# Kernel tuning notes

Measured on AMD Instinct MI355X. Metric: run time of the kernel, lower is better.

## Reference

```python
import jax, jax.numpy as jnp
import numpy as np

B, S, D_IN, D_OUT = 4, 2048, 1024, 1024
USE_MASK = True


def setup_inputs() -> dict:
    key = jax.random.key(0)
    ks = jax.random.split(key, 6)
    return {
        "inputs_for_keys": jax.random.normal(ks[0], (B, S, D_IN), jnp.float32),
        "inputs_for_values": jax.random.normal(ks[1], (B, S, D_IN), jnp.float32),
        "inputs_for_queries": jax.random.normal(ks[2], (B, S, D_IN), jnp.float32),
        "WK": jax.random.normal(ks[3], (D_IN, D_OUT), jnp.float32) * 0.1,
        "WV": jax.random.normal(ks[4], (D_IN, D_OUT), jnp.float32) * 0.1,
        "WQ": jax.random.normal(ks[5], (D_IN, D_OUT), jnp.float32) * 0.1,
    }


def reference(inputs_for_keys, inputs_for_values, inputs_for_queries, WK, WV, WQ):
    # projections: [B,S,Din] @ [Din,Dout] -> [B,S,Dout]
    K = jnp.einsum("bsd,de->bse", inputs_for_keys, WK)
    V = jnp.einsum("bsd,de->bse", inputs_for_values, WV)
    Q = jnp.einsum("bsd,de->bse", inputs_for_queries, WQ)

    dk = jnp.asarray(K.shape[2], jnp.float32)
    # scores: [B, Sq, Sk]
    score = jnp.einsum("bqd,bkd->bqk", Q, K) / jnp.sqrt(dk)
    if USE_MASK:
        # causal: -inf strictly above diagonal (j > i), matching the
        # transposed tril(-1) * -inf construction in the original.
        q_idx = jnp.arange(S)[:, None]
        k_idx = jnp.arange(S)[None, :]
        mask = jnp.where(k_idx > q_idx, -jnp.inf, 0.0).astype(score.dtype)
        score = score + mask[None, :, :]
    soft_score = jax.nn.softmax(score, axis=-1)
    return jnp.einsum("bqk,bkd->bqd", soft_score, V)
```

## Files before the change

### kernel.cpp

```cpp
#include <hip/hip_runtime.h>
#include <hip/hip_bf16.h>

typedef unsigned short u16;
typedef _Float16 f16;
typedef __attribute__((ext_vector_type(8))) short s16x8;
typedef __attribute__((ext_vector_type(8))) _Float16 f16x8;
typedef __attribute__((ext_vector_type(4))) float f32x4;
typedef __attribute__((ext_vector_type(4))) unsigned short u16x4;

template <typename T>
__device__ __forceinline__ auto mfma_try(T a, T b, f32x4 c, int)
    -> decltype(__builtin_amdgcn_mfma_f32_16x16x32_f16(a, b, c, 0, 0, 0)) {
  return __builtin_amdgcn_mfma_f32_16x16x32_f16(a, b, c, 0, 0, 0);
}
template <typename T>
__device__ __forceinline__ f32x4 mfma_try(T a, T b, f32x4 c, long) {
  return __builtin_amdgcn_mfma_f32_16x16x32_f16(
      __builtin_bit_cast(f16x8, a), __builtin_bit_cast(f16x8, b), c, 0, 0, 0);
}
__device__ __forceinline__ f32x4 MFMA16(s16x8 a, s16x8 b, f32x4 c) {
  return mfma_try(a, b, c, 0);
}

__device__ __forceinline__ void gload16(const void* g, void* s) {
  __builtin_amdgcn_global_load_lds(
      (const __attribute__((address_space(1))) void*)g,
      (__attribute__((address_space(3))) void*)s, 16, 0, 0);
}

__device__ __forceinline__ u16 f2h(float x) {
  f16 h = (f16)x;
  u16 u;
  __builtin_memcpy(&u, &h, 2);
  return u;
}
__device__ __forceinline__ float h2f(u16 u) {
  f16 h;
  __builtin_memcpy(&h, &u, 2);
  return (float)h;
}

#define LDS_SWZ(r, cb) ((cb) ^ (((r)&7) << 4))

struct Geom {
  int srow[4], scol[4];
  int w, l, wr, wc;
};

__device__ __forceinline__ Geom make_geom() {
  Geom g;
  int tid = threadIdx.x;
  g.w = tid >> 6; g.l = tid & 63;
  g.wr = g.w >> 1; g.wc = g.w & 1;
#pragma unroll
  for (int i = 0; i < 4; ++i) {
    int off = i * 4096 + g.w * 1024 + g.l * 16;
    int r = off >> 7, cb = off & 127;
    g.srow[i] = r;
    g.scol[i] = LDS_SWZ(r, cb) >> 1;
  }
  return g;
}

__device__ __forceinline__ void stage(const u16* pan, int ld, int k0,
                                      char* lds, const Geom& g) {
#pragma unroll
  for (int i = 0; i < 4; ++i)
    gload16(pan + (long)g.srow[i] * ld + k0 + g.scol[i],
            lds + i * 4096 + g.w * 1024);
}

__device__ __forceinline__ void compute_step(const char* lA, const char* lB,
                                             const Geom& g, f32x4 acc[4][4]) {
#pragma unroll
  for (int ks = 0; ks < 2; ++ks) {
    s16x8 af[4], bg[4];
#pragma unroll
    for (int m = 0; m < 4; ++m) {
      int r = g.wr * 64 + m * 16 + (g.l & 15);
      int cb = ks * 64 + ((g.l >> 4) << 4);
      af[m] = *(const s16x8*)(lA + r * 128 + LDS_SWZ(r, cb));
    }
#pragma unroll
    for (int n = 0; n < 4; ++n) {
      int r = g.wc * 64 + n * 16 + (g.l & 15);
      int cb = ks * 64 + ((g.l >> 4) << 4);
      bg[n] = *(const s16x8*)(lB + r * 128 + LDS_SWZ(r, cb));
    }
#pragma unroll
    for (int m = 0; m < 4; ++m)
#pragma unroll
      for (int n = 0; n < 4; ++n)
        acc[m][n] = MFMA16(af[m], bg[n], acc[m][n]);
  }
}

__device__ __forceinline__ void gemm_core(const u16* Apan, int lda,
                                          const u16* Bpan, int ldb, int nsteps,
                                          char* lA, char* lB, const Geom& g,
                                          f32x4 acc[4][4]) {
  stage(Apan, lda, 0, lA, g);
  stage(Bpan, ldb, 0, lB, g);
  __syncthreads();
  for (int t = 0; t < nsteps; ++t) {
    int cur = (t & 1) << 14;
    if (t + 1 < nsteps) {
      int nxt = ((t + 1) & 1) << 14;
      stage(Apan, lda, (t + 1) * 64, lA + nxt, g);
      stage(Bpan, ldb, (t + 1) * 64, lB + nxt, g);
    }
    compute_step(lA + cur, lB + cur, g, acc);
    if (t + 1 < nsteps) __syncthreads();
  }
}

__global__ __launch_bounds__(256, 2) void proj_kernel(
    const u16* __restrict__ xk, const u16* __restrict__ xq, const u16* __restrict__ xv,
    const u16* __restrict__ wk, const u16* __restrict__ wq, const u16* __restrict__ wv,
    u16* __restrict__ K, u16* __restrict__ Q, u16* __restrict__ Vt) {
  __shared__ char lds[65536];
  const int y = blockIdx.y;
  const u16* X = y == 0 ? xk : (y == 1 ? xq : xv);
  const u16* W = y == 0 ? wk : (y == 1 ? wq : wv);
  const int bx = blockIdx.x;
  const int swz = (bx & 7) * 64 + (bx >> 3);
  const int tm = swz >> 3, tn = swz & 7;
  Geom g = make_geom();
  f32x4 acc[4][4] = {};
  gemm_core(X + (long)tm * 128 * 1024, 1024, W + (long)tn * 128 * 1024, 1024,
            16, lds, lds + 32768, g, acc);
  const int rg0 = tm * 128 + g.wr * 64, cg0 = tn * 128 + g.wc * 64;
  if (y < 2) {
    u16* C = y == 0 ? K : Q;
#pragma unroll
    for (int m = 0; m < 4; ++m)
#pragma unroll
      for (int n = 0; n < 4; ++n)
#pragma unroll
        for (int j = 0; j < 4; ++j) {
          int rg = rg0 + m * 16 + ((g.l >> 4) << 2) + j;
          int cg = cg0 + n * 16 + (g.l & 15);
          C[(long)rg * 1024 + cg] = f2h(acc[m][n][j]);
        }
  } else {
#pragma unroll
    for (int m = 0; m < 4; ++m) {
      int rg = rg0 + m * 16 + ((g.l >> 4) << 2);
      int b = rg >> 11, rl = rg & 2047;
#pragma unroll
      for (int n = 0; n < 4; ++n) {
        int cg = cg0 + n * 16 + (g.l & 15);
        u16x4 pk;
#pragma unroll
        for (int j = 0; j < 4; ++j) pk[j] = f2h(acc[m][n][j]);
        *(u16x4*)(Vt + (long)b * (1024 * 2048) + (long)cg * 2048 + rl) = pk;
      }
    }
  }
}

__global__ __launch_bounds__(256, 2) void qkt_kernel(
    const u16* __restrict__ Q, const u16* __restrict__ K, u16* __restrict__ S) {
  __shared__ char lds[65536];
  const int bx = blockIdx.x;
  const int swz = (bx & 7) * 68 + (bx >> 3);
  const int b = swz / 136;
  int t = swz - b * 136;
  int tm = 0;
  while (t > tm) { t -= tm + 1; ++tm; }
  const int tn = t;
  Geom g = make_geom();
  f32x4 acc[4][4] = {};
  const u16* Qb = Q + (long)b * 2048 * 1024;
  const u16* Kb = K + (long)b * 2048 * 1024;
  gemm_core(Qb + (long)tm * 128 * 1024, 1024, Kb + (long)tn * 128 * 1024, 1024,
            16, lds, lds + 32768, g, acc);
  u16* Sb = S + (long)b * 2048 * 2048;
  const int rg0 = tm * 128 + g.wr * 64, cg0 = tn * 128 + g.wc * 64;
#pragma unroll
  for (int m = 0; m < 4; ++m)
#pragma unroll
    for (int n = 0; n < 4; ++n)
#pragma unroll
      for (int j = 0; j < 4; ++j) {
        int rg = rg0 + m * 16 + ((g.l >> 4) << 2) + j;
        int cg = cg0 + n * 16 + (g.l & 15);
        Sb[(long)rg * 2048 + cg] = f2h(acc[m][n][j]);
      }
}

__global__ __launch_bounds__(256, 2) void pv_kernel(
    const u16* __restrict__ P, const u16* __restrict__ Vt, float* __restrict__ O) {
  __shared__ char lds[65536];
  const int bx = blockIdx.x;
  const int swz = (bx & 7) * 64 + (bx >> 3);
  const int b = swz >> 7, loc = swz & 127;
  const int tm = loc >> 3, tn = loc & 7;
  Geom g = make_geom();
  f32x4 acc[4][4] = {};
  gemm_core(P + ((long)b * 2048 + tm * 128) * 2048, 2048,
            Vt + (long)b * 1024 * 2048 + (long)tn * 128 * 2048, 2048,
            (tm + 1) * 2, lds, lds + 32768, g, acc);
  const int rg0 = tm * 128 + g.wr * 64, cg0 = tn * 128 + g.wc * 64;
#pragma unroll
  for (int m = 0; m < 4; ++m)
#pragma unroll
    for (int n = 0; n < 4; ++n)
#pragma unroll
      for (int j = 0; j < 4; ++j) {
        int rg = rg0 + m * 16 + ((g.l >> 4) << 2) + j;
        int cg = cg0 + n * 16 + (g.l & 15);
        O[((long)b * 2048 + rg) * 1024 + cg] = acc[m][n][j];
      }
}

__global__ __launch_bounds__(256) void softmax_causal(
    const u16* __restrict__ S, u16* __restrict__ P) {
  const int row = blockIdx.x;
  const int i_q = row & 2047;
  const u16* sr = S + (long)row * 2048;
  u16* pr = P + (long)row * 2048;
  const int tid = threadIdx.x;
  const int l = tid & 63, w = tid >> 6;
  const int base = tid * 8;

  s16x8 raw = *(const s16x8*)(sr + base);
  float v[8];
  float m = -INFINITY;
#pragma unroll
  for (int j = 0; j < 8; ++j) {
    float x = h2f((u16)raw[j]);
    x = (base + j <= i_q) ? x : -INFINITY;
    v[j] = x;
    m = fmaxf(m, x);
  }
  __shared__ float red[8];
  for (int o = 32; o; o >>= 1) m = fmaxf(m, __shfl_xor(m, o, 64));
  if (l == 0) red[w] = m;
  __syncthreads();
  m = fmaxf(fmaxf(red[0], red[1]), fmaxf(red[2], red[3]));

  float s = 0.f;
#pragma unroll
  for (int j = 0; j < 8; ++j) {
    v[j] = expf(v[j] - m);
    s += v[j];
  }
  for (int o = 32; o; o >>= 1) s += __shfl_xor(s, o, 64);
  if (l == 0) red[4 + w] = s;
  __syncthreads();
  s = (red[4] + red[5]) + (red[6] + red[7]);
  float inv = 1.0f / s;

  s16x8 o;
#pragma unroll
  for (int j = 0; j < 8; ++j) o[j] = (short)f2h(v[j] * inv);
  *(s16x8*)(pr + base) = o;
}

__global__ __launch_bounds__(256) void xcast_kernel(
    const float* __restrict__ x0, const float* __restrict__ x1,
    const float* __restrict__ x2, u16* __restrict__ o0, u16* __restrict__ o1,
    u16* __restrict__ o2) {
  const int y = blockIdx.y;
  const float* in = y == 0 ? x0 : (y == 1 ? x1 : x2);
  u16* out = y == 0 ? o0 : (y == 1 ? o1 : o2);
  long i = ((long)blockIdx.x * 256 + threadIdx.x) * 8;
  f32x4 a = *(const f32x4*)(in + i);
  f32x4 b = *(const f32x4*)(in + i + 4);
  s16x8 o;
#pragma unroll
  for (int j = 0; j < 4; ++j) {
    o[j] = (short)f2h(a[j]);
    o[4 + j] = (short)f2h(b[j]);
  }
  *(s16x8*)(out + i) = o;
}

__global__ __launch_bounds__(256) void wcast_kernel(
    const float* __restrict__ wk, const float* __restrict__ wv,
    const float* __restrict__ wq, u16* __restrict__ ok, u16* __restrict__ ov,
    u16* __restrict__ oq) {
  __shared__ float tile[32][33];
  const int z = blockIdx.z;
  const float* w = z == 0 ? wk : (z == 1 ? wv : wq);
  u16* o = z == 0 ? ok : (z == 1 ? ov : oq);
  const float scale = (z == 2) ? 0.03125f : 1.0f;
  const int bx = blockIdx.x, by = blockIdx.y;
  const int lx = threadIdx.x & 31, ly = threadIdx.x >> 5;
#pragma unroll
  for (int j = 0; j < 32; j += 8)
    tile[ly + j][lx] = w[(long)(by * 32 + ly + j) * 1024 + bx * 32 + lx];
  __syncthreads();
#pragma unroll
  for (int j = 0; j < 32; j += 8)
    o[(long)(bx * 32 + ly + j) * 1024 + by * 32 + lx] = f2h(tile[lx][ly + j] * scale);
}

extern "C" void kernel_launch(void* const* d_in, const int* in_sizes, int n_in,
                              void* d_out, int out_size, void* d_ws, size_t ws_size,
                              hipStream_t stream) {
  const float* Xk = (const float*)d_in[0];
  const float* Xv = (const float*)d_in[1];
  const float* Xq = (const float*)d_in[2];
  const float* WK = (const float*)d_in[3];
  const float* WV = (const float*)d_in[4];
  const float* WQ = (const float*)d_in[5];

  const int Bn = 4, S = 2048, D = 1024;
  const long NX = (long)Bn * S * D;

  const size_t r0 = (size_t)Bn * S * S * 4;
  const size_t r1 = r0 + 3ull * D * D * 2;
  const size_t r2 = r1 + 2ull * NX * 2;
  const size_t NEED = r2 + (size_t)NX * 2;
  if (ws_size < NEED) {
    hipMemsetAsync(d_out, 0, (size_t)out_size * 4, stream);
    return;
  }
  char* ws = (char*)d_ws;
  u16* xkb = (u16*)ws;
  u16* xvb = xkb + NX;
  u16* xqb = xvb + NX;
  u16* scoresH = (u16*)ws;
  u16* wkt = (u16*)(ws + r0);
  u16* wvt = wkt + D * D;
  u16* wqt = wvt + D * D;
  u16* Kb = (u16*)(ws + r1);
  u16* Qb = Kb + NX;
  u16* Pb = (u16*)(ws + r1);
  u16* Vt = (u16*)(ws + r2);

  xcast_kernel<<<dim3(4096, 3), 256, 0, stream>>>(Xk, Xv, Xq, xkb, xvb, xqb);
  wcast_kernel<<<dim3(32, 32, 3), 256, 0, stream>>>(WK, WV, WQ, wkt, wvt, wqt);
  proj_kernel<<<dim3(512, 3), 256, 0, stream>>>(xkb, xqb, xvb, wkt, wqt, wvt,
                                                Kb, Qb, Vt);
  qkt_kernel<<<dim3(544), 256, 0, stream>>>(Qb, Kb, scoresH);
  softmax_causal<<<dim3(8192), 256, 0, stream>>>(scoresH, Pb);
  pv_kernel<<<dim3(512), 256, 0, stream>>>(Pb, Vt, (float*)d_out);
}
```

Baseline: 163.4 us.

## Use 256x256 tiles with 8-wave pipelined GEMM for projection and QK^T

Replaces the 128x128, 4-wave GEMM used by the projection and score kernels with a 256x256 tile, 8-wave core. The new core double-buffers 64 KB LDS stages, splits global-to-LDS loads into halves that are issued between MFMA quarters, and uses explicit waitcnt, barriers and setprio. The goal is higher operand reuse and better overlap of loads with MFMA work. In exchange there are far fewer blocks (144 for QK^T), much larger LDS use, and possible tail or occupancy loss.

After: 171.7 us. 1.05x slower.

```diff
diff --git a/kernel.cpp b/kernel.cpp
--- a/kernel.cpp
+++ b/kernel.cpp
@@ -41,6 +41,183 @@
 }
 
 #define LDS_SWZ(r, cb) ((cb) ^ (((r)&7) << 4))
+
+__device__ __forceinline__ void bar() { __builtin_amdgcn_s_barrier(); }
+__device__ __forceinline__ void lgkm0() {
+  asm volatile("s_waitcnt lgkmcnt(0)" ::: "memory");
+  __builtin_amdgcn_sched_barrier(0);
+}
+__device__ __forceinline__ void vm4() {
+  asm volatile("s_waitcnt vmcnt(4)" ::: "memory");
+}
+__device__ __forceinline__ void vm0() {
+  asm volatile("s_waitcnt vmcnt(0)" ::: "memory");
+}
+
+__device__ __forceinline__ void gemm256_core(
+    const u16* __restrict__ Apan, int lda, const u16* __restrict__ Bpan,
+    int ldb, int ns, char* lds, f32x4 (&acc)[8][4]) {
+  const int tid = threadIdx.x;
+  const int w = tid >> 6, l = tid & 63;
+  const int wr = w >> 2, wc = w & 3;
+
+  const int sr = tid >> 3;
+  const int scol = (((tid & 7) * 16) ^ ((sr & 7) << 4)) >> 1;
+
+  auto stageH = [&](const u16* pan, int ld, int t, int h, int region) {
+    char* dst = lds + ((t & 1) << 16) + region * 16384 + (w << 10);
+    const u16* src = pan + (long)(h * 128 + sr) * ld + t * 64 + scol;
+    gload16(src, dst);
+    gload16(src + (long)64 * ld, dst + 8192);
+  };
+  auto rdA = [&](int p, int m, int ks) -> s16x8 {
+    int r = m * 16 + (l & 15);
+    int cb = ks * 64 + ((l >> 4) << 4);
+    return *(const s16x8*)(lds + (p << 16) + wr * 16384 + r * 128 + LDS_SWZ(r, cb));
+  };
+  auto rdB = [&](int p, int n, int ks) -> s16x8 {
+    int row = wc * 64 + n * 16 + (l & 15);
+    int r = row & 127;
+    int cb = ks * 64 + ((l >> 4) << 4);
+    return *(const s16x8*)(lds + (p << 16) + (2 + (wc >> 1)) * 16384 + r * 128 +
+                           LDS_SWZ(r, cb));
+  };
+
+  stageH(Apan, lda, 0, 0, 0);
+  stageH(Apan, lda, 0, 1, 1);
+  stageH(Bpan, ldb, 0, 0, 2);
+  stageH(Bpan, ldb, 0, 1, 3);
+  if (ns > 1) {
+    stageH(Apan, lda, 1, 0, 0);
+    stageH(Apan, lda, 1, 1, 1);
+    vm4();
+  } else {
+    vm0();
+  }
+  bar();
+
+  for (int t = 0; t < ns; ++t) {
+    const int p = t & 1;
+    s16x8 af[8][2], bf[4][2];
+    auto do_mfma = [&](int mb) {
+#pragma unroll
+      for (int m = 0; m < 2; ++m)
+#pragma unroll
+        for (int n = 0; n < 4; ++n) {
+          acc[mb + m][n] = MFMA16(af[mb + m][0], bf[n][0], acc[mb + m][n]);
+          acc[mb + m][n] = MFMA16(af[mb + m][1], bf[n][1], acc[mb + m][n]);
+        }
+    };
+#pragma unroll
+    for (int n = 0; n < 4; ++n) { bf[n][0] = rdB(p, n, 0); bf[n][1] = rdB(p, n, 1); }
+#pragma unroll
+    for (int m = 0; m < 2; ++m) { af[m][0] = rdA(p, m, 0); af[m][1] = rdA(p, m, 1); }
+    if (t + 1 < ns) stageH(Bpan, ldb, t + 1, 0, 2);
+    bar(); lgkm0();
+    __builtin_amdgcn_s_setprio(1);
+    do_mfma(0);
+    __builtin_amdgcn_s_setprio(0);
+    bar();
+#pragma unroll
+    for (int m = 2; m < 8; ++m) { af[m][0] = rdA(p, m, 0); af[m][1] = rdA(p, m, 1); }
+    if (t + 1 < ns) stageH(Bpan, ldb, t + 1, 1, 3);
+    bar(); lgkm0();
+    __builtin_amdgcn_s_setprio(1);
+    do_mfma(2);
+    __builtin_amdgcn_s_setprio(0);
+    bar();
+    if (t + 2 < ns) stageH(Apan, lda, t + 2, 0, 0);
+    bar(); lgkm0();
+    __builtin_amdgcn_s_setprio(1);
+    do_mfma(4);
+    __builtin_amdgcn_s_setprio(0);
+    bar();
+    if (t + 2 < ns) stageH(Apan, lda, t + 2, 1, 1);
+    bar(); lgkm0();
+    __builtin_amdgcn_s_setprio(1);
+    do_mfma(6);
+    __builtin_amdgcn_s_setprio(0);
+    if (t + 2 < ns) vm4(); else vm0();
+    bar();
+  }
+}
+
+__global__ __launch_bounds__(512, 2) void proj256_kernel(
+    const u16* __restrict__ xk, const u16* __restrict__ xq, const u16* __restrict__ xv,
+    const u16* __restrict__ wk, const u16* __restrict__ wq, const u16* __restrict__ wv,
+    u16* __restrict__ K, u16* __restrict__ Q, u16* __restrict__ Vt) {
+  __shared__ char lds[131072];
+  const int y = blockIdx.y;
+  const u16* X = y == 0 ? xk : (y == 1 ? xq : xv);
+  const u16* W = y == 0 ? wk : (y == 1 ? wq : wv);
+  const int bx = blockIdx.x;
+  const int swz = (bx & 7) * 16 + (bx >> 3);
+  const int tm = swz >> 2, tn = swz & 3;
+  f32x4 acc[8][4] = {};
+  gemm256_core(X + (long)tm * 256 * 1024, 1024, W + (long)tn * 256 * 1024, 1024,
+               16, lds, acc);
+  const int l = threadIdx.x & 63, w = threadIdx.x >> 6;
+  const int wr = w >> 2, wc = w & 3;
+  const int rg0 = tm * 256 + wr * 128, cg0 = tn * 256 + wc * 64;
+  if (y < 2) {
+    u16* C = y == 0 ? K : Q;
+#pragma unroll
+    for (int m = 0; m < 8; ++m)
+#pragma unroll
+      for (int n = 0; n < 4; ++n)
+#pragma unroll
+        for (int j = 0; j < 4; ++j) {
+          int rg = rg0 + m * 16 + ((l >> 4) << 2) + j;
+          int cg = cg0 + n * 16 + (l & 15);
+          C[(long)rg * 1024 + cg] = f2h(acc[m][n][j]);
+        }
+  } else {
+#pragma unroll
+    for (int m = 0; m < 8; ++m) {
+      int rg = rg0 + m * 16 + ((l >> 4) << 2);
+      int b = rg >> 11, rl = rg & 2047;
+#pragma unroll
+      for (int n = 0; n < 4; ++n) {
+        int cg = cg0 + n * 16 + (l & 15);
+        u16x4 pk;
+#pragma unroll
+        for (int j = 0; j < 4; ++j) pk[j] = f2h(acc[m][n][j]);
+        *(u16x4*)(Vt + (long)b * (1024 * 2048) + (long)cg * 2048 + rl) = pk;
+      }
+    }
+  }
+}
+
+__global__ __launch_bounds__(512, 2) void qkt256_kernel(
+    const u16* __restrict__ Q, const u16* __restrict__ K, u16* __restrict__ S) {
+  __shared__ char lds[131072];
+  const int bx = blockIdx.x;
+  const int swz = (bx & 7) * 18 + (bx >> 3);
+  const int b = swz / 36;
+  int t = swz - b * 36;
+  int tm = 0;
+  while (t > tm) { t -= tm + 1; ++tm; }
+  const int tn = t;
+  f32x4 acc[8][4] = {};
+  const u16* Qb = Q + (long)b * 2048 * 1024;
+  const u16* Kb = K + (long)b * 2048 * 1024;
+  gemm256_core(Qb + (long)tm * 256 * 1024, 1024, Kb + (long)tn * 256 * 1024,
+               1024, 16, lds, acc);
+  u16* Sb = S + (long)b * 2048 * 2048;
+  const int l = threadIdx.x & 63, w = threadIdx.x >> 6;
+  const int wr = w >> 2, wc = w & 3;
+  const int rg0 = tm * 256 + wr * 128, cg0 = tn * 256 + wc * 64;
+#pragma unroll
+  for (int m = 0; m < 8; ++m)
+#pragma unroll
+    for (int n = 0; n < 4; ++n)
+#pragma unroll
+      for (int j = 0; j < 4; ++j) {
+        int rg = rg0 + m * 16 + ((l >> 4) << 2) + j;
+        int cg = cg0 + n * 16 + (l & 15);
+        Sb[(long)rg * 2048 + cg] = f2h(acc[m][n][j]);
+      }
+}
 
 struct Geom {
   int srow[4], scol[4];
@@ -114,81 +291,6 @@
   }
 }
 
-__global__ __launch_bounds__(256, 2) void proj_kernel(
-    const u16* __restrict__ xk, const u16* __restrict__ xq, const u16* __restrict__ xv,
-    const u16* __restrict__ wk, const u16* __restrict__ wq, const u16* __restrict__ wv,
-    u16* __restrict__ K, u16* __restrict__ Q, u16* __restrict__ Vt) {
-  __shared__ char lds[65536];
-  const int y = blockIdx.y;
-  const u16* X = y == 0 ? xk : (y == 1 ? xq : xv);
-  const u16* W = y == 0 ? wk : (y == 1 ? wq : wv);
-  const int bx = blockIdx.x;
-  const int swz = (bx & 7) * 64 + (bx >> 3);
-  const int tm = swz >> 3, tn = swz & 7;
-  Geom g = make_geom();
-  f32x4 acc[4][4] = {};
-  gemm_core(X + (long)tm * 128 * 1024, 1024, W + (long)tn * 128 * 1024, 1024,
-            16, lds, lds + 32768, g, acc);
-  const int rg0 = tm * 128 + g.wr * 64, cg0 = tn * 128 + g.wc * 64;
-  if (y < 2) {
-    u16* C = y == 0 ? K : Q;
-#pragma unroll
-    for (int m = 0; m < 4; ++m)
-#pragma unroll
-      for (int n = 0; n < 4; ++n)
-#pragma unroll
-        for (int j = 0; j < 4; ++j) {
-          int rg = rg0 + m * 16 + ((g.l >> 4) << 2) + j;
-          int cg = cg0 + n * 16 + (g.l & 15);
-          C[(long)rg * 1024 + cg] = f2h(acc[m][n][j]);
-        }
-  } else {
-#pragma unroll
-    for (int m = 0; m < 4; ++m) {
-      int rg = rg0 + m * 16 + ((g.l >> 4) << 2);
-      int b = rg >> 11, rl = rg & 2047;
-#pragma unroll
-      for (int n = 0; n < 4; ++n) {
-        int cg = cg0 + n * 16 + (g.l & 15);
-        u16x4 pk;
-#pragma unroll
-        for (int j = 0; j < 4; ++j) pk[j] = f2h(acc[m][n][j]);
-        *(u16x4*)(Vt + (long)b * (1024 * 2048) + (long)cg * 2048 + rl) = pk;
-      }
-    }
-  }
-}
-
-__global__ __launch_bounds__(256, 2) void qkt_kernel(
-    const u16* __restrict__ Q, const u16* __restrict__ K, u16* __restrict__ S) {
-  __shared__ char lds[65536];
-  const int bx = blockIdx.x;
-  const int swz = (bx & 7) * 68 + (bx >> 3);
-  const int b = swz / 136;
-  int t = swz - b * 136;
-  int tm = 0;
-  while (t > tm) { t -= tm + 1; ++tm; }
-  const int tn = t;
-  Geom g = make_geom();
-  f32x4 acc[4][4] = {};
-  const u16* Qb = Q + (long)b * 2048 * 1024;
-  const u16* Kb = K + (long)b * 2048 * 1024;
-  gemm_core(Qb + (long)tm * 128 * 1024, 1024, Kb + (long)tn * 128 * 1024, 1024,
-            16, lds, lds + 32768, g, acc);
-  u16* Sb = S + (long)b * 2048 * 2048;
-  const int rg0 = tm * 128 + g.wr * 64, cg0 = tn * 128 + g.wc * 64;
-#pragma unroll
-  for (int m = 0; m < 4; ++m)
-#pragma unroll
-    for (int n = 0; n < 4; ++n)
-#pragma unroll
-      for (int j = 0; j < 4; ++j) {
-        int rg = rg0 + m * 16 + ((g.l >> 4) << 2) + j;
-        int cg = cg0 + n * 16 + (g.l & 15);
-        Sb[(long)rg * 2048 + cg] = f2h(acc[m][n][j]);
-      }
-}
-
 __global__ __launch_bounds__(256, 2) void pv_kernel(
     const u16* __restrict__ P, const u16* __restrict__ Vt, float* __restrict__ O) {
   __shared__ char lds[65536];
@@ -333,9 +435,9 @@
 
   xcast_kernel<<<dim3(4096, 3), 256, 0, stream>>>(Xk, Xv, Xq, xkb, xvb, xqb);
   wcast_kernel<<<dim3(32, 32, 3), 256, 0, stream>>>(WK, WV, WQ, wkt, wvt, wqt);
-  proj_kernel<<<dim3(512, 3), 256, 0, stream>>>(xkb, xqb, xvb, wkt, wqt, wvt,
-                                                Kb, Qb, Vt);
-  qkt_kernel<<<dim3(544), 256, 0, stream>>>(Qb, Kb, scoresH);
+  proj256_kernel<<<dim3(128, 3), 512, 0, stream>>>(xkb, xqb, xvb, wkt, wqt, wvt,
+                                                   Kb, Qb, Vt);
+  qkt256_kernel<<<dim3(144), 512, 0, stream>>>(Qb, Kb, scoresH);
   softmax_causal<<<dim3(8192), 256, 0, stream>>>(scoresH, Pb);
   pv_kernel<<<dim3(512), 256, 0, stream>>>(Pb, Vt, (float*)d_out);
 }
```
